# Kernel tuning notes

Measured on AMD Instinct MI355X. Metric: run time of the kernel, lower is better.

## Reference

```python
import jax, jax.numpy as jnp
import numpy as np
import math

WINDOW = 2048
EMBED = 1024
BATCH = 8


def setup_inputs() -> dict:
    key = jax.random.key(0)
    ks = jax.random.split(key, 7)
    s = 1.0 / math.sqrt(EMBED)
    return {
        "embeddings": jax.random.normal(ks[0], (BATCH, WINDOW, EMBED), dtype=jnp.float32),
        "Wq": jax.random.uniform(ks[1], (EMBED, EMBED), jnp.float32, -s, s),
        "bq": jax.random.uniform(ks[2], (EMBED,), jnp.float32, -s, s),
        "Wk": jax.random.uniform(ks[3], (EMBED, EMBED), jnp.float32, -s, s),
        "bk": jax.random.uniform(ks[4], (EMBED,), jnp.float32, -s, s),
        "Wv": jax.random.uniform(ks[5], (EMBED, EMBED), jnp.float32, -s, s),
        "bv": jax.random.uniform(ks[6], (EMBED,), jnp.float32, -s, s),
    }


def reference(embeddings, Wq, bq, Wk, bk, Wv, bv):
    # Linear layers: x @ W.T + b (torch nn.Linear convention)
    Q = jnp.einsum('bse,fe->bsf', embeddings, Wq) + bq
    K = jnp.einsum('bse,fe->bsf', embeddings, Wk) + bk
    V = jnp.einsum('bse,fe->bsf', embeddings, Wv) + bv
    scale = 1.0 / math.sqrt(EMBED)
    # [B, S, S] score matrix: A[b, i, j] = Q_i . K_j / sqrt(d)
    A = jnp.einsum('bie,bje->bij', Q, K) * scale
    # causal additive mask: -inf where j > i (strictly upper triangular)
    mask = jnp.triu(jnp.full((WINDOW, WINDOW), -jnp.inf, dtype=A.dtype), k=1)
    A = A + mask
    # NOTE: faithful to original nn.Softmax(dim=1): normalize over QUERY axis
    P = jax.nn.softmax(A, axis=1)
    return jnp.einsum('bij,bje->bie', P, V)
```

## Files before the change

kernel.cpp:

```cpp
#include <hip/hip_runtime.h>
#include <stdint.h>

#define WINDOW 2048
#define EMBED  1024
#define BATCH  8
#define MTOT   (BATCH*WINDOW)

typedef unsigned short u16;
typedef __bf16 bf16x8 __attribute__((ext_vector_type(8)));
typedef float  f32x4  __attribute__((ext_vector_type(4)));

#define BK 64
#define KSCALE 0.04508422717564447f

#define BM2 256
#define BN2 256
#define HALF2 8192

#define WAITVM4 asm volatile("s_waitcnt vmcnt(4)" ::: "memory")
#define WAITVM0 asm volatile("s_waitcnt vmcnt(0)" ::: "memory")
#define SBAR    __builtin_amdgcn_s_barrier()

__device__ __forceinline__ u16 f2bf(float f) {
  union { float f; unsigned u; } a; a.f = f;
  unsigned r = a.u + 0x7FFF + ((a.u >> 16) & 1);
  return (u16)(r >> 16);
}
__device__ __forceinline__ float bf2f(u16 u) {
  union { unsigned u; float f; } a; a.u = ((unsigned)u) << 16;
  return a.f;
}

__device__ __forceinline__ void gload16(const u16* g, u16* l) {
  __builtin_amdgcn_global_load_lds(
      (const __attribute__((address_space(1))) unsigned int*)g,
      (__attribute__((address_space(3))) unsigned int*)l, 16, 0, 0);
}


__device__ __forceinline__ void gemm256(
    const u16* __restrict__ A, int lda,
    const u16* __restrict__ B, int ldb,
    int nt, u16* lds, f32x4 acc[8][4])
{
  const int tid  = threadIdx.x;
  const int lane = tid & 63;
  const int wid  = tid >> 6;
  const int wm   = (wid >> 2) * 128;
  const int wn   = (wid & 3) * 64;
  const int lrow = lane & 15;
  const int hi   = lane >> 4;
  u16* dA = lds;
  u16* dB = lds + 4 * HALF2;

  int aoff[8], boff[4];
  #pragma unroll
  for (int mi = 0; mi < 8; ++mi) {
    int r = wm + mi * 16 + lrow;
    aoff[mi] = r * 32 + ((hi ^ ((r >> 1) & 3)) << 3);
  }
  #pragma unroll
  for (int ni = 0; ni < 4; ++ni) {
    int r = wn + ni * 16 + lrow;
    boff[ni] = r * 32 + ((hi ^ ((r >> 1) & 3)) << 3);
  }

  const int f0 = tid, f1 = 512 + tid;
  const int r0 = f0 >> 2, r1 = f1 >> 2;
  const int c0 = (((f0 & 3) ^ ((r0 >> 1) & 3)) << 3);
  const int c1 = (((f1 & 3) ^ ((r1 >> 1) & 3)) << 3);
  const u16* pA0 = A + (size_t)r0 * lda + c0;
  const u16* pA1 = A + (size_t)r1 * lda + c1;
  const u16* pB0 = B + (size_t)r0 * ldb + c0;
  const u16* pB1 = B + (size_t)r1 * ldb + c1;
  const int d0 = f0 * 8, d1 = f1 * 8;

  gload16(pA0,      dA + d0);         gload16(pA1,      dA + d1);
  gload16(pB0,      dB + d0);         gload16(pB1,      dB + d1);
  gload16(pA0 + 32, dA + HALF2 + d0); gload16(pA1 + 32, dA + HALF2 + d1);
  gload16(pB0 + 32, dB + HALF2 + d0); gload16(pB1 + 32, dB + HALF2 + d1);
  pA0 += BK; pA1 += BK; pB0 += BK; pB1 += BK;
  WAITVM4;
  SBAR;

  for (int t = 0; t < nt; ++t) {
    const int cb = (t & 1) * 2;
    const int nb = ((t + 1) & 1) * 2;
    u16* LA0 = dA + cb * HALF2;  u16* LA1 = LA0 + HALF2;
    u16* LB0 = dB + cb * HALF2;  u16* LB1 = LB0 + HALF2;
    const bool s = (t + 1) < nt;
    bf16x8 av[4], bv[4];

    #pragma unroll
    for (int mi = 0; mi < 4; ++mi) av[mi] = *(const bf16x8*)(LA0 + aoff[mi]);
    #pragma unroll
    for (int ni = 0; ni < 4; ++ni) bv[ni] = *(const bf16x8*)(LB0 + boff[ni]);
    if (s) { gload16(pA0, dA + nb * HALF2 + d0); gload16(pA1, dA + nb * HALF2 + d1); }
    __builtin_amdgcn_s_setprio(1);
    #pragma unroll
    for (int mi = 0; mi < 4; ++mi)
      #pragma unroll
      for (int ni = 0; ni < 4; ++ni)
        acc[mi][ni] = __builtin_amdgcn_mfma_f32_16x16x32_bf16(av[mi], bv[ni], acc[mi][ni], 0, 0, 0);
    __builtin_amdgcn_s_setprio(0);
    SBAR;

    #pragma unroll
    for (int mi = 0; mi < 4; ++mi) av[mi] = *(const bf16x8*)(LA0 + aoff[4 + mi]);
    if (s) { gload16(pB0, dB + nb * HALF2 + d0); gload16(pB1, dB + nb * HALF2 + d1); }
    __builtin_amdgcn_s_setprio(1);
    #pragma unroll
    for (int mi = 0; mi < 4; ++mi)
      #pragma unroll
      for (int ni = 0; ni < 4; ++ni)
        acc[4 + mi][ni] = __builtin_amdgcn_mfma_f32_16x16x32_bf16(av[mi], bv[ni], acc[4 + mi][ni], 0, 0, 0);
    __builtin_amdgcn_s_setprio(0);
    if (s) { WAITVM4; } else { WAITVM0; }
    SBAR;

    #pragma unroll
    for (int mi = 0; mi < 4; ++mi) av[mi] = *(const bf16x8*)(LA1 + aoff[mi]);
    #pragma unroll
    for (int ni = 0; ni < 4; ++ni) bv[ni] = *(const bf16x8*)(LB1 + boff[ni]);
    if (s) { gload16(pA0 + 32, dA + nb * HALF2 + HALF2 + d0); gload16(pA1 + 32, dA + nb * HALF2 + HALF2 + d1); }
    __builtin_amdgcn_s_setprio(1);
    #pragma unroll
    for (int mi = 0; mi < 4; ++mi)
      #pragma unroll
      for (int ni = 0; ni < 4; ++ni)
        acc[mi][ni] = __builtin_amdgcn_mfma_f32_16x16x32_bf16(av[mi], bv[ni], acc[mi][ni], 0, 0, 0);
    __builtin_amdgcn_s_setprio(0);
    SBAR;

    #pragma unroll
    for (int mi = 0; mi < 4; ++mi) av[mi] = *(const bf16x8*)(LA1 + aoff[4 + mi]);
    if (s) {
      gload16(pB0 + 32, dB + nb * HALF2 + HALF2 + d0); gload16(pB1 + 32, dB + nb * HALF2 + HALF2 + d1);
      pA0 += BK; pA1 += BK; pB0 += BK; pB1 += BK;
    }
    __builtin_amdgcn_s_setprio(1);
    #pragma unroll
    for (int mi = 0; mi < 4; ++mi)
      #pragma unroll
      for (int ni = 0; ni < 4; ++ni)
        acc[4 + mi][ni] = __builtin_amdgcn_mfma_f32_16x16x32_bf16(av[mi], bv[ni], acc[4 + mi][ni], 0, 0, 0);
    __builtin_amdgcn_s_setprio(0);
    if (s) { WAITVM4; }
    SBAR;
  }
}

__global__ __launch_bounds__(256) void k_cvt(const float* __restrict__ in,
                                             u16* __restrict__ out, int n) {
  int i = (blockIdx.x * 256 + threadIdx.x) * 4;
  if (i >= n) return;
  float4 v = *(const float4*)(in + i);
  ushort4 o;
  o.x = f2bf(v.x); o.y = f2bf(v.y); o.z = f2bf(v.z); o.w = f2bf(v.w);
  *(ushort4*)(out + i) = o;
}

__global__ __launch_bounds__(512, 2) void k_qkv(
    const u16* __restrict__ Xb, const u16* __restrict__ Wb,
    const float* __restrict__ bq, const float* __restrict__ bk, const float* __restrict__ bv,
    u16* __restrict__ Q, u16* __restrict__ Ks, u16* __restrict__ V)
{
  __shared__ u16 lds[8 * HALF2];
  const int m0 = blockIdx.x * BM2;
  const int n0 = blockIdx.y * BN2;
  const int z  = blockIdx.z;
  const u16*   W    = Wb + (size_t)z * EMBED * EMBED;
  const float* bias = (z == 0) ? bq : (z == 1) ? bk : bv;
  u16* out          = (z == 0) ? Q  : (z == 1) ? Ks : V;
  const float scale = (z == 1) ? KSCALE : 1.0f;

  f32x4 acc[8][4];
  const f32x4 zz = {0.f,0.f,0.f,0.f};
  #pragma unroll
  for (int i = 0; i < 8; ++i) for (int j = 0; j < 4; ++j) acc[i][j] = zz;
  gemm256(Xb + (size_t)m0 * EMBED, EMBED, W + (size_t)n0 * EMBED, EMBED,
          EMBED / BK, lds, acc);

  const int lane = threadIdx.x & 63, wid = threadIdx.x >> 6;
  const int wm = (wid >> 2) * 128, wn = (wid & 3) * 64;
  const int lrow = lane & 15, hi = lane >> 4;
  #pragma unroll
  for (int mi = 0; mi < 8; ++mi)
    #pragma unroll
    for (int ni = 0; ni < 4; ++ni)
      #pragma unroll
      for (int rr = 0; rr < 4; ++rr) {
        int gm = m0 + wm + mi * 16 + hi * 4 + rr;
        int gn = n0 + wn + ni * 16 + lrow;
        out[(size_t)gm * EMBED + gn] = f2bf((acc[mi][ni][rr] + bias[gn]) * scale);
      }
}

__global__ __launch_bounds__(512, 2) void k_spd(
    const u16* __restrict__ Q, const u16* __restrict__ Ks,
    u16* __restrict__ P, float* __restrict__ D)
{
  const int i0 = blockIdx.x * BM2;
  const int j0 = blockIdx.y * BN2;
  if (j0 > i0) return;
  const int b  = blockIdx.z;
  __shared__ u16 lds[8 * HALF2];
  const u16* A = Q  + (size_t)b * WINDOW * EMBED + (size_t)i0 * EMBED;
  const u16* B = Ks + (size_t)b * WINDOW * EMBED + (size_t)j0 * EMBED;
  f32x4 acc[8][4];
  const f32x4 zz = {0.f,0.f,0.f,0.f};
  #pragma unroll
  for (int i = 0; i < 8; ++i) for (int j = 0; j < 4; ++j) acc[i][j] = zz;
  gemm256(A, EMBED, B, EMBED, EMBED / BK, lds, acc);

  u16* Pb   = P + (size_t)b * WINDOW * WINDOW;
  float* Db = D + (size_t)b * WINDOW;
  const int lane = threadIdx.x & 63, wid = threadIdx.x >> 6;
  const int wm = (wid >> 2) * 128, wn = (wid & 3) * 64;
  const int lrow = lane & 15, hi = lane >> 4;
  #pragma unroll
  for (int ni = 0; ni < 4; ++ni) {
    int gj = j0 + wn + ni * 16 + lrow;
    float csum = 0.f;
    #pragma unroll
    for (int mi = 0; mi < 8; ++mi)
      #pragma unroll
      for (int rr = 0; rr < 4; ++rr) {
        int gi = i0 + wm + mi * 16 + hi * 4 + rr;
        float p = (gi >= gj) ? exp2f(acc[mi][ni][rr]) : 0.0f;
        Pb[(size_t)gi * WINDOW + gj] = f2bf(p);
        csum += p;
      }
    csum += __shfl_xor(csum, 16, 64);
    csum += __shfl_xor(csum, 32, 64);
    if (hi == 0) atomicAdd(&Db[gj], csum);
  }
}

__global__ __launch_bounds__(256) void k_vdt(
    const u16* __restrict__ V, const float* __restrict__ D, u16* __restrict__ Vdt)
{
  __shared__ u16 tile[64][68];
  const int j0 = blockIdx.x * 64, e0 = blockIdx.y * 64, b = blockIdx.z;
  const u16* Vb = V   + (size_t)b * WINDOW * EMBED;
  u16* Tb       = Vdt + (size_t)b * EMBED * WINDOW;
  const float* Db = D + (size_t)b * WINDOW;
  const int t = threadIdx.x;
  const int rr = t >> 4;
  const int cc = (t & 15) * 4;
  #pragma unroll
  for (int p = 0; p < 4; ++p) {
    int r = p * 16 + rr;
    *(uint2*)&tile[r][cc] = *(const uint2*)(Vb + (size_t)(j0 + r) * EMBED + e0 + cc);
  }
  __syncthreads();
  #pragma unroll
  for (int p = 0; p < 4; ++p) {
    int er = p * 16 + rr;
    ushort4 o;
    o.x = f2bf(bf2f(tile[cc + 0][er]) / Db[j0 + cc + 0]);
    o.y = f2bf(bf2f(tile[cc + 1][er]) / Db[j0 + cc + 1]);
    o.z = f2bf(bf2f(tile[cc + 2][er]) / Db[j0 + cc + 2]);
    o.w = f2bf(bf2f(tile[cc + 3][er]) / Db[j0 + cc + 3]);
    *(ushort4*)(Tb + (size_t)(e0 + er) * WINDOW + j0 + cc) = o;
  }
}

__global__ __launch_bounds__(512, 2) void k_out(
    const u16* __restrict__ P, const u16* __restrict__ Vdt, float* __restrict__ O)
{
  __shared__ u16 lds[8 * HALF2];
  const int i0 = ((int)gridDim.x - 1 - (int)blockIdx.x) * BM2;
  const int e0 = blockIdx.y * BN2;
  const int b  = blockIdx.z;
  const u16* A = P   + (size_t)b * WINDOW * WINDOW + (size_t)i0 * WINDOW;
  const u16* B = Vdt + (size_t)b * EMBED * WINDOW  + (size_t)e0 * WINDOW;
  f32x4 acc[8][4];
  const f32x4 zz = {0.f,0.f,0.f,0.f};
  #pragma unroll
  for (int i = 0; i < 8; ++i) for (int j = 0; j < 4; ++j) acc[i][j] = zz;
  gemm256(A, WINDOW, B, WINDOW, (i0 + BM2) / BK, lds, acc);

  float* Ob = O + (size_t)b * WINDOW * EMBED;
  const int lane = threadIdx.x & 63, wid = threadIdx.x >> 6;
  const int wm = (wid >> 2) * 128, wn = (wid & 3) * 64;
  const int lrow = lane & 15, hi = lane >> 4;
  #pragma unroll
  for (int mi = 0; mi < 8; ++mi)
    #pragma unroll
    for (int ni = 0; ni < 4; ++ni)
      #pragma unroll
      for (int rr = 0; rr < 4; ++rr) {
        int gi = i0 + wm + mi * 16 + hi * 4 + rr;
        int ge = e0 + wn + ni * 16 + lrow;
        Ob[(size_t)gi * EMBED + ge] = acc[mi][ni][rr];
      }
}

extern "C" void kernel_launch(void* const* d_in, const int* in_sizes, int n_in,
                              void* d_out, int out_size, void* d_ws, size_t ws_size,
                              hipStream_t stream) {
  const float* X  = (const float*)d_in[0];
  const float* Wq = (const float*)d_in[1];
  const float* bq = (const float*)d_in[2];
  const float* Wk = (const float*)d_in[3];
  const float* bk = (const float*)d_in[4];
  const float* Wv = (const float*)d_in[5];
  const float* bv = (const float*)d_in[6];
  float* O = (float*)d_out;

  char* ws = (char*)d_ws;
  size_t off = 0;
  auto alloc = [&](size_t bytes) -> void* {
    void* p = ws + off; off += (bytes + 255) & ~(size_t)255; return p;
  };
  u16*  Xb  = (u16*)alloc((size_t)MTOT * EMBED * 2);
  u16*  Wb  = (u16*)alloc((size_t)3 * EMBED * EMBED * 2);
  u16*  Qb  = (u16*)alloc((size_t)MTOT * EMBED * 2);
  u16*  Kb  = (u16*)alloc((size_t)MTOT * EMBED * 2);
  u16*  Vb  = (u16*)alloc((size_t)MTOT * EMBED * 2);
  u16*  Vdt = (u16*)alloc((size_t)BATCH * EMBED * WINDOW * 2);
  u16*  P   = (u16*)alloc((size_t)BATCH * WINDOW * WINDOW * 2);
  float* D  = (float*)alloc((size_t)MTOT * 4);
  (void)ws_size; (void)in_sizes; (void)n_in; (void)out_size;

  k_cvt<<<dim3((MTOT * EMBED / 4 + 255) / 256), 256, 0, stream>>>(X, Xb, MTOT * EMBED);
  k_cvt<<<dim3((EMBED * EMBED / 4 + 255) / 256), 256, 0, stream>>>(Wq, Wb, EMBED * EMBED);
  k_cvt<<<dim3((EMBED * EMBED / 4 + 255) / 256), 256, 0, stream>>>(Wk, Wb + (size_t)EMBED * EMBED, EMBED * EMBED);
  k_cvt<<<dim3((EMBED * EMBED / 4 + 255) / 256), 256, 0, stream>>>(Wv, Wb + (size_t)2 * EMBED * EMBED, EMBED * EMBED);

  k_qkv<<<dim3(MTOT / BM2, EMBED / BN2, 3), 512, 0, stream>>>(Xb, Wb, bq, bk, bv, Qb, Kb, Vb);

  (void)hipMemsetAsync(D, 0, (size_t)MTOT * 4, stream);
  k_spd<<<dim3(WINDOW / BM2, WINDOW / BN2, BATCH), 512, 0, stream>>>(Qb, Kb, P, D);

  k_vdt<<<dim3(WINDOW / 64, EMBED / 64, BATCH), 256, 0, stream>>>(Vb, D, Vdt);

  k_out<<<dim3(WINDOW / BM2, EMBED / BN2, BATCH), 512, 0, stream>>>(P, Vdt, O);
}
```

Before: 301.2 us.

## Software-pipeline LDS fragment loads, merge weight conversions, remap QKV grid per XCD

```diff
diff --git a/kernel.cpp b/kernel.cpp
--- a/kernel.cpp
+++ b/kernel.cpp
@@ -18,6 +18,7 @@
 #define HALF2 8192
 
 #define WAITVM4 asm volatile("s_waitcnt vmcnt(4)" ::: "memory")
+#define WAITVM2 asm volatile("s_waitcnt vmcnt(2)" ::: "memory")
 #define WAITVM0 asm volatile("s_waitcnt vmcnt(0)" ::: "memory")
 #define SBAR    __builtin_amdgcn_s_barrier()
 
@@ -83,19 +84,21 @@
   WAITVM4;
   SBAR;
 
+  bf16x8 av[4], bv[4];
+  #pragma unroll
+  for (int mi = 0; mi < 4; ++mi) av[mi] = *(const bf16x8*)(dA + aoff[mi]);
+  #pragma unroll
+  for (int ni = 0; ni < 4; ++ni) bv[ni] = *(const bf16x8*)(dB + boff[ni]);
+
   for (int t = 0; t < nt; ++t) {
     const int cb = (t & 1) * 2;
     const int nb = ((t + 1) & 1) * 2;
     u16* LA0 = dA + cb * HALF2;  u16* LA1 = LA0 + HALF2;
     u16* LB0 = dB + cb * HALF2;  u16* LB1 = LB0 + HALF2;
+    u16* NA0 = dA + nb * HALF2;  u16* NB0 = dB + nb * HALF2;
     const bool s = (t + 1) < nt;
-    bf16x8 av[4], bv[4];
-
-    #pragma unroll
-    for (int mi = 0; mi < 4; ++mi) av[mi] = *(const bf16x8*)(LA0 + aoff[mi]);
-    #pragma unroll
-    for (int ni = 0; ni < 4; ++ni) bv[ni] = *(const bf16x8*)(LB0 + boff[ni]);
-    if (s) { gload16(pA0, dA + nb * HALF2 + d0); gload16(pA1, dA + nb * HALF2 + d1); }
+
+    SBAR;
     __builtin_amdgcn_s_setprio(1);
     #pragma unroll
     for (int mi = 0; mi < 4; ++mi)
@@ -104,10 +107,11 @@
         acc[mi][ni] = __builtin_amdgcn_mfma_f32_16x16x32_bf16(av[mi], bv[ni], acc[mi][ni], 0, 0, 0);
     __builtin_amdgcn_s_setprio(0);
     SBAR;
-
     #pragma unroll
     for (int mi = 0; mi < 4; ++mi) av[mi] = *(const bf16x8*)(LA0 + aoff[4 + mi]);
-    if (s) { gload16(pB0, dB + nb * HALF2 + d0); gload16(pB1, dB + nb * HALF2 + d1); }
+    if (s) { gload16(pA0, NA0 + d0); gload16(pA1, NA0 + d1); }
+
+    SBAR;
     __builtin_amdgcn_s_setprio(1);
     #pragma unroll
     for (int mi = 0; mi < 4; ++mi)
@@ -115,14 +119,15 @@
       for (int ni = 0; ni < 4; ++ni)
         acc[4 + mi][ni] = __builtin_amdgcn_mfma_f32_16x16x32_bf16(av[mi], bv[ni], acc[4 + mi][ni], 0, 0, 0);
     __builtin_amdgcn_s_setprio(0);
-    if (s) { WAITVM4; } else { WAITVM0; }
-    SBAR;
-
+    if (s) { WAITVM2; } else { WAITVM0; }
+    SBAR;
     #pragma unroll
     for (int mi = 0; mi < 4; ++mi) av[mi] = *(const bf16x8*)(LA1 + aoff[mi]);
     #pragma unroll
     for (int ni = 0; ni < 4; ++ni) bv[ni] = *(const bf16x8*)(LB1 + boff[ni]);
-    if (s) { gload16(pA0 + 32, dA + nb * HALF2 + HALF2 + d0); gload16(pA1 + 32, dA + nb * HALF2 + HALF2 + d1); }
+    if (s) { gload16(pB0, NB0 + d0); gload16(pB1, NB0 + d1); }
+
+    SBAR;
     __builtin_amdgcn_s_setprio(1);
     #pragma unroll
     for (int mi = 0; mi < 4; ++mi)
@@ -131,13 +136,11 @@
         acc[mi][ni] = __builtin_amdgcn_mfma_f32_16x16x32_bf16(av[mi], bv[ni], acc[mi][ni], 0, 0, 0);
     __builtin_amdgcn_s_setprio(0);
     SBAR;
-
     #pragma unroll
     for (int mi = 0; mi < 4; ++mi) av[mi] = *(const bf16x8*)(LA1 + aoff[4 + mi]);
-    if (s) {
-      gload16(pB0 + 32, dB + nb * HALF2 + HALF2 + d0); gload16(pB1 + 32, dB + nb * HALF2 + HALF2 + d1);
-      pA0 += BK; pA1 += BK; pB0 += BK; pB1 += BK;
-    }
+    if (s) { gload16(pA0 + 32, NA0 + HALF2 + d0); gload16(pA1 + 32, NA0 + HALF2 + d1); }
+
+    SBAR;
     __builtin_amdgcn_s_setprio(1);
     #pragma unroll
     for (int mi = 0; mi < 4; ++mi)
@@ -145,8 +148,16 @@
       for (int ni = 0; ni < 4; ++ni)
         acc[4 + mi][ni] = __builtin_amdgcn_mfma_f32_16x16x32_bf16(av[mi], bv[ni], acc[4 + mi][ni], 0, 0, 0);
     __builtin_amdgcn_s_setprio(0);
-    if (s) { WAITVM4; }
-    SBAR;
+    if (s) { WAITVM2; }
+    SBAR;
+    if (s) {
+      #pragma unroll
+      for (int mi = 0; mi < 4; ++mi) av[mi] = *(const bf16x8*)(NA0 + aoff[mi]);
+      #pragma unroll
+      for (int ni = 0; ni < 4; ++ni) bv[ni] = *(const bf16x8*)(NB0 + boff[ni]);
+      gload16(pB0 + 32, NB0 + HALF2 + d0); gload16(pB1 + 32, NB0 + HALF2 + d1);
+      pA0 += BK; pA1 += BK; pB0 += BK; pB1 += BK;
+    }
   }
 }
 
@@ -160,15 +171,33 @@
   *(ushort4*)(out + i) = o;
 }
 
+__global__ __launch_bounds__(256) void k_cvtw(const float* __restrict__ w0,
+                                              const float* __restrict__ w1,
+                                              const float* __restrict__ w2,
+                                              u16* __restrict__ out) {
+  const float* in = (blockIdx.y == 0) ? w0 : (blockIdx.y == 1) ? w1 : w2;
+  u16* o = out + (size_t)blockIdx.y * EMBED * EMBED;
+  int i = (blockIdx.x * 256 + threadIdx.x) * 4;
+  float4 v = *(const float4*)(in + i);
+  ushort4 r;
+  r.x = f2bf(v.x); r.y = f2bf(v.y); r.z = f2bf(v.z); r.w = f2bf(v.w);
+  *(ushort4*)(o + i) = r;
+}
+
 __global__ __launch_bounds__(512, 2) void k_qkv(
     const u16* __restrict__ Xb, const u16* __restrict__ Wb,
     const float* __restrict__ bq, const float* __restrict__ bk, const float* __restrict__ bv,
     u16* __restrict__ Q, u16* __restrict__ Ks, u16* __restrict__ V)
 {
   __shared__ u16 lds[8 * HALF2];
-  const int m0 = blockIdx.x * BM2;
-  const int n0 = blockIdx.y * BN2;
-  const int z  = blockIdx.z;
+  const int bid   = blockIdx.x;
+  const int xcd   = bid & 7;
+  const int g     = bid >> 3;
+  const int mloc  = g & 7;
+  const int combo = g >> 3;
+  const int m0 = (xcd * 8 + mloc) * BM2;
+  const int n0 = (combo & 3) * BN2;
+  const int z  = combo >> 2;
   const u16*   W    = Wb + (size_t)z * EMBED * EMBED;
   const float* bias = (z == 0) ? bq : (z == 1) ? bk : bv;
   u16* out          = (z == 0) ? Q  : (z == 1) ? Ks : V;
@@ -325,11 +354,9 @@
   (void)ws_size; (void)in_sizes; (void)n_in; (void)out_size;
 
   k_cvt<<<dim3((MTOT * EMBED / 4 + 255) / 256), 256, 0, stream>>>(X, Xb, MTOT * EMBED);
-  k_cvt<<<dim3((EMBED * EMBED / 4 + 255) / 256), 256, 0, stream>>>(Wq, Wb, EMBED * EMBED);
-  k_cvt<<<dim3((EMBED * EMBED / 4 + 255) / 256), 256, 0, stream>>>(Wk, Wb + (size_t)EMBED * EMBED, EMBED * EMBED);
-  k_cvt<<<dim3((EMBED * EMBED / 4 + 255) / 256), 256, 0, stream>>>(Wv, Wb + (size_t)2 * EMBED * EMBED, EMBED * EMBED);
-
-  k_qkv<<<dim3(MTOT / BM2, EMBED / BN2, 3), 512, 0, stream>>>(Xb, Wb, bq, bk, bv, Qb, Kb, Vb);
+  k_cvtw<<<dim3(EMBED * EMBED / 4 / 256, 3), 256, 0, stream>>>(Wq, Wk, Wv, Wb);
+
+  k_qkv<<<dim3(768), 512, 0, stream>>>(Xb, Wb, bq, bk, bv, Qb, Kb, Vb);
 
   (void)hipMemsetAsync(D, 0, (size_t)MTOT * 4, stream);
   k_spd<<<dim3(WINDOW / BM2, WINDOW / BN2, BATCH), 512, 0, stream>>>(Qb, Kb, P, D);
```

Measured after the change: 298.2 us. About the same (-1.0%).
